# Kernel tuning notes

Hardware: AMD Instinct MI355X
Metric: run time of the kernel (lower is better)

Reference implementation:

```python
import jax, jax.numpy as jnp
import numpy as np

B, S, H = 32, 512, 2048
FP, SP = 1024, 1024


def setup_inputs() -> dict:
    key = jax.random.key(0)
    ks = jax.random.split(key, 8)
    X = jax.random.normal(ks[0], (B, S, H), dtype=jnp.float32)
    pY = jax.random.randint(ks[1], (B, S), 0, 3)
    # Y must be consistent with pY: hcw rows index [2, 2+FP), roo rows [2+FP, 2+FP+SP)
    y_hcw = jax.random.randint(ks[2], (B, S), 2, 2 + FP)
    y_roo = jax.random.randint(ks[3], (B, S), 2 + FP, 2 + FP + SP)
    Y = jnp.where(pY == 1, y_hcw, jnp.where(pY == 2, y_roo, 0))
    sc = 1.0 / np.sqrt(H)
    W_end = jax.random.normal(ks[4], (1, H), dtype=jnp.float32) * sc
    b_end = jnp.zeros((1,), jnp.float32)
    W_hcw = jax.random.normal(ks[5], (FP, H), dtype=jnp.float32) * sc
    b_hcw = jnp.zeros((FP,), jnp.float32)
    W_roo = jax.random.normal(ks[6], (SP, H), dtype=jnp.float32) * sc
    b_roo = jnp.zeros((SP,), jnp.float32)
    return {"X": X, "pY": pY, "Y": Y, "W_end": W_end, "b_end": b_end,
            "W_hcw": W_hcw, "b_hcw": b_hcw, "W_roo": W_roo, "b_roo": b_roo}


def reference(X, pY, Y, W_end, b_end, W_hcw, b_hcw, W_roo, b_roo):
    b, s, h = X.shape
    N = b * s
    Xf = X.reshape(N, h)
    pYf = pY.reshape(N)
    Yf = Y.reshape(N)

    end_mask = pYf == 0
    hcw_mask = pYf == 1
    roo_mask = pYf == 2

    # end head (Bernoulli prob)
    end_logit = Xf @ W_end.T + b_end            # [N, 1]
    end_prob = jax.nn.sigmoid(end_logit)[:, 0]  # [N]
    non_end = 1.0 - end_prob

    # hcw / roo heads: dense compute over all tokens, masked results match
    # the torch gather/scatter exactly at valid positions.
    P_hcw = jax.nn.softmax(Xf @ W_hcw.T + b_hcw, axis=-1)  # [N, FP]
    P_roo = jax.nn.softmax(Xf @ W_roo.T + b_roo, axis=-1)  # [N, SP]

    fp = W_hcw.shape[0]
    sp = W_roo.shape[0]
    idx_hcw = jnp.clip(Yf - 2, 0, fp - 1)
    idx_roo = jnp.clip(Yf - 2 - fp, 0, sp - 1)
    prob_hcw = jnp.take_along_axis(P_hcw, idx_hcw[:, None], axis=1)[:, 0]
    prob_roo = jnp.take_along_axis(P_roo, idx_roo[:, None], axis=1)[:, 0]

    prob = jnp.where(end_mask, end_prob,
                     jnp.where(hcw_mask, prob_hcw * non_end,
                               jnp.where(roo_mask, prob_roo * non_end, 1.0)))

    em = end_mask.astype(X.dtype)[:, None]
    hm = hcw_mask.astype(X.dtype)[:, None]
    rm = roo_mask.astype(X.dtype)[:, None]
    col_end = jnp.broadcast_to(end_prob[:, None], (N, 2)) * em        # [N, 2]
    col_hcw = P_hcw * non_end[:, None] * hm                           # [N, FP]
    col_roo = P_roo * non_end[:, None] * rm                           # [N, SP]
    prob_all_mat = jnp.concatenate([col_end, col_hcw, col_roo], axis=-1)

    log_prob = jnp.log(prob)
    return log_prob.reshape(b, s), prob_all_mat.reshape(b, s, fp + sp + 2)
```

## Files before the change

kernel.cpp:

```cpp
#include <hip/hip_runtime.h>
#include <hip/hip_bf16.h>
#include <cstddef>
#include <cstdint>

#define N_TOK 16384
#define H_    2048
#define FP_   1024
#define SP_   1024
#define C_    2050

#define BM 128
#define BN 128
#define BK 64
#define KP 72

typedef short bf16x8 __attribute__((ext_vector_type(8)));
typedef float f32x4  __attribute__((ext_vector_type(4)));
typedef float f4     __attribute__((ext_vector_type(4)));
typedef float f2     __attribute__((ext_vector_type(2)));

__device__ __forceinline__ unsigned pack_bf2(float a, float b) {
  __hip_bfloat16 x = __float2bfloat16(a);
  __hip_bfloat16 y = __float2bfloat16(b);
  unsigned short ux, uy;
  __builtin_memcpy(&ux, &x, 2);
  __builtin_memcpy(&uy, &y, 2);
  return (unsigned)ux | ((unsigned)uy << 16);
}

__device__ __forceinline__ unsigned short f2bf(float f) {
  __hip_bfloat16 h = __float2bfloat16(f);
  unsigned short u;
  __builtin_memcpy(&u, &h, 2);
  return u;
}

__device__ __forceinline__ float bf2f(unsigned short u) {
  unsigned v = (unsigned)u << 16;
  float f;
  __builtin_memcpy(&f, &v, 4);
  return f;
}

__global__ __launch_bounds__(256) void convert_kernel(
    const float* __restrict__ X,
    const float* __restrict__ W_hcw, const float* __restrict__ W_roo,
    const float* __restrict__ W_end, const float* __restrict__ b_end,
    unsigned short* __restrict__ Xb, unsigned short* __restrict__ Wb,
    float* __restrict__ mat)
{
  const int wave = threadIdx.x >> 6;
  const int lane = threadIdx.x & 63;
  const int row  = (blockIdx.x << 2) + wave;
  const bool isX = row < N_TOK;
  const float* src;
  unsigned short* dst;
  if (isX) {
    src = X + (size_t)row * H_;
    dst = Xb + (size_t)row * H_;
  } else {
    const int m = row - N_TOK;
    src = (m < FP_) ? (W_hcw + (size_t)m * H_) : (W_roo + (size_t)(m - FP_) * H_);
    dst = Wb + (size_t)m * H_;
  }
  float s = 0.f;
#pragma unroll
  for (int i = 0; i < 8; ++i) {
    const int e = (lane << 2) + (i << 8);
    f4 v = __builtin_nontemporal_load((const f4*)(src + e));
    uint2 p;
    p.x = pack_bf2(v[0], v[1]);
    p.y = pack_bf2(v[2], v[3]);
    *(uint2*)(dst + e) = p;
    if (isX) {
      float4 w = *(const float4*)(W_end + e);
      s += v[0] * w.x + v[1] * w.y + v[2] * w.z + v[3] * w.w;
    }
  }
  if (isX) {
#pragma unroll
    for (int o = 32; o; o >>= 1) s += __shfl_xor(s, o);
    if (lane == 0) mat[(size_t)row * C_] = s + b_end[0];
  }
}

__global__ __launch_bounds__(256) void gemm_lds_kernel(
    const unsigned short* __restrict__ Xb, const unsigned short* __restrict__ Wb,
    const float* __restrict__ b_hcw, const float* __restrict__ b_roo,
    float* __restrict__ mat)
{
  __shared__ __align__(16) unsigned short As[BM * BK];
  __shared__ __align__(16) unsigned short Bs[BN * BK];

  const int bid = blockIdx.x;
  const int xcd = bid & 7;
  const int loc = bid >> 3;
  const int c0 = (((xcd << 1) | (loc & 1))) * BN;
  const int n0 = (loc >> 1) * BM;
  const float* bias = (c0 < FP_) ? (b_hcw + c0) : (b_roo + (c0 - FP_));

  const int t    = threadIdx.x;
  const int wave = t >> 6;
  const int lane = t & 63;
  const int wy   = wave >> 1;
  const int wx   = wave & 1;
  const int quad = lane >> 4;
  const int l16  = lane & 15;

  const int srow   = t >> 3;
  const int gchunk = (t & 7) ^ (srow & 7);
  const unsigned short* gA = Xb + (size_t)(n0 + srow) * H_ + (gchunk << 3);
  const unsigned short* gB = Wb + (size_t)(c0 + srow) * H_ + (gchunk << 3);

  f32x4 acc[4][4];
#pragma unroll
  for (int i = 0; i < 4; ++i)
#pragma unroll
    for (int j = 0; j < 4; ++j)
#pragma unroll
      for (int r = 0; r < 4; ++r) acc[i][j][r] = 0.f;

  for (int k0 = 0; k0 < H_; k0 += BK) {
#pragma unroll
    for (int r = 0; r < 4; ++r) {
      __builtin_amdgcn_global_load_lds(
          (const __attribute__((address_space(1))) unsigned int*)(gA + (size_t)(r * 32) * H_ + k0),
          (__attribute__((address_space(3))) unsigned int*)(&As[(r * 32 + srow) * BK + ((t & 7) << 3)]),
          16, 0, 0);
      __builtin_amdgcn_global_load_lds(
          (const __attribute__((address_space(1))) unsigned int*)(gB + (size_t)(r * 32) * H_ + k0),
          (__attribute__((address_space(3))) unsigned int*)(&Bs[(r * 32 + srow) * BK + ((t & 7) << 3)]),
          16, 0, 0);
    }
    __syncthreads();

#pragma unroll
    for (int kk = 0; kk < 2; ++kk) {
      bf16x8 af[4], bfr[4];
      const int sw = l16 & 7;
#pragma unroll
      for (int i = 0; i < 4; ++i) {
        const int pos = ((kk << 2) + quad) ^ sw;
        af[i] = *(const bf16x8*)&As[(wy * 64 + i * 16 + l16) * BK + (pos << 3)];
      }
#pragma unroll
      for (int j = 0; j < 4; ++j) {
        const int pos = ((kk << 2) + quad) ^ sw;
        bfr[j] = *(const bf16x8*)&Bs[(wx * 64 + j * 16 + l16) * BK + (pos << 3)];
      }
#pragma unroll
      for (int i = 0; i < 4; ++i)
#pragma unroll
        for (int j = 0; j < 4; ++j)
          acc[i][j] = __builtin_amdgcn_mfma_f32_16x16x32_bf16(af[i], bfr[j], acc[i][j], 0, 0, 0);
    }
    __syncthreads();
  }

  float bj[4];
#pragma unroll
  for (int j = 0; j < 4; ++j) bj[j] = bias[wx * 64 + j * 16 + l16];
#pragma unroll
  for (int i = 0; i < 4; ++i) {
#pragma unroll
    for (int r = 0; r < 4; ++r) {
      const int row = n0 + wy * 64 + i * 16 + quad * 4 + r;
      unsigned short* dst =
          (unsigned short*)(mat + (size_t)row * C_ + 4) + c0 + wx * 64 + l16;
#pragma unroll
      for (int j = 0; j < 4; ++j) dst[j * 16] = f2bf(acc[i][j][r] + bj[j]);
    }
  }
}

__global__ __launch_bounds__(256) void end_head_kernel(
    const float* __restrict__ X, const float* __restrict__ W_end,
    const float* __restrict__ b_end, float* __restrict__ mat)
{
  const int wave = threadIdx.x >> 6;
  const int lane = threadIdx.x & 63;
  const int n = (blockIdx.x << 2) + wave;
  const float* x = X + (size_t)n * H_;
  float s = 0.f;
#pragma unroll
  for (int i = 0; i < 8; ++i) {
    const int e = (lane + (i << 6)) << 2;
    float4 xv = *(const float4*)(x + e);
    float4 wv = *(const float4*)(W_end + e);
    s += xv.x * wv.x + xv.y * wv.y + xv.z * wv.z + xv.w * wv.w;
  }
#pragma unroll
  for (int o = 32; o; o >>= 1) s += __shfl_xor(s, o);
  if (lane == 0) mat[(size_t)n * C_] = s + b_end[0];
}

__global__ __launch_bounds__(256) void logits_gemm_fused(
    const float* __restrict__ X,
    const float* __restrict__ W_hcw, const float* __restrict__ W_roo,
    const float* __restrict__ b_hcw, const float* __restrict__ b_roo,
    float* __restrict__ mat)
{
  __shared__ __align__(16) unsigned short As[BM * KP];
  __shared__ __align__(16) unsigned short Bs[BN * KP];

  const int c0 = blockIdx.x * BN;
  const int n0 = blockIdx.y * BM;
  const float* Wbase = (c0 < FP_) ? (W_hcw + (size_t)c0 * H_)
                                  : (W_roo + (size_t)(c0 - FP_) * H_);
  const float* bias  = (c0 < FP_) ? (b_hcw + c0) : (b_roo + (c0 - FP_));

  const int t    = threadIdx.x;
  const int wave = t >> 6;
  const int lane = t & 63;
  const int wy   = wave >> 1;
  const int wx   = wave & 1;
  const int quad = lane >> 4;
  const int l16  = lane & 15;
  const int tq = t & 3;
  const int tr = t >> 2;

  f32x4 acc[4][4];
#pragma unroll
  for (int i = 0; i < 4; ++i)
#pragma unroll
    for (int j = 0; j < 4; ++j)
#pragma unroll
      for (int r = 0; r < 4; ++r) acc[i][j][r] = 0.f;

  for (int k0 = 0; k0 < H_; k0 += BK) {
#pragma unroll
    for (int p = 0; p < 2; ++p) {
      const int row = tr + (p << 6);
      const float4* xs = (const float4*)(X + (size_t)(n0 + row) * H_ + k0 + (tq << 4));
      const float4* ws = (const float4*)(Wbase + (size_t)row * H_ + k0 + (tq << 4));
      float4 x0 = xs[0], x1 = xs[1], x2 = xs[2], x3 = xs[3];
      float4 w0 = ws[0], w1 = ws[1], w2 = ws[2], w3 = ws[3];
      uint4 ua0 = {pack_bf2(x0.x, x0.y), pack_bf2(x0.z, x0.w),
                   pack_bf2(x1.x, x1.y), pack_bf2(x1.z, x1.w)};
      uint4 ua1 = {pack_bf2(x2.x, x2.y), pack_bf2(x2.z, x2.w),
                   pack_bf2(x3.x, x3.y), pack_bf2(x3.z, x3.w)};
      uint4 ub0 = {pack_bf2(w0.x, w0.y), pack_bf2(w0.z, w0.w),
                   pack_bf2(w1.x, w1.y), pack_bf2(w1.z, w1.w)};
      uint4 ub1 = {pack_bf2(w2.x, w2.y), pack_bf2(w2.z, w2.w),
                   pack_bf2(w3.x, w3.y), pack_bf2(w3.z, w3.w)};
      *(uint4*)&As[row * KP + (tq << 4)]     = ua0;
      *(uint4*)&As[row * KP + (tq << 4) + 8] = ua1;
      *(uint4*)&Bs[row * KP + (tq << 4)]     = ub0;
      *(uint4*)&Bs[row * KP + (tq << 4) + 8] = ub1;
    }
    __syncthreads();
#pragma unroll
    for (int kk = 0; kk < 2; ++kk) {
      bf16x8 af[4], bfr[4];
#pragma unroll
      for (int i = 0; i < 4; ++i)
        af[i] = *(const bf16x8*)&As[(wy * 64 + i * 16 + l16) * KP + kk * 32 + quad * 8];
#pragma unroll
      for (int j = 0; j < 4; ++j)
        bfr[j] = *(const bf16x8*)&Bs[(wx * 64 + j * 16 + l16) * KP + kk * 32 + quad * 8];
#pragma unroll
      for (int i = 0; i < 4; ++i)
#pragma unroll
        for (int j = 0; j < 4; ++j)
          acc[i][j] = __builtin_amdgcn_mfma_f32_16x16x32_bf16(af[i], bfr[j], acc[i][j], 0, 0, 0);
    }
    __syncthreads();
  }

  float bj[4];
#pragma unroll
  for (int j = 0; j < 4; ++j) bj[j] = bias[wx * 64 + j * 16 + l16];
#pragma unroll
  for (int i = 0; i < 4; ++i) {
#pragma unroll
    for (int r = 0; r < 4; ++r) {
      const int row = n0 + wy * 64 + i * 16 + quad * 4 + r;
      unsigned short* dst =
          (unsigned short*)(mat + (size_t)row * C_ + 4) + c0 + wx * 64 + l16;
#pragma unroll
      for (int j = 0; j < 4; ++j) dst[j * 16] = f2bf(acc[i][j][r] + bj[j]);
    }
  }
}

__global__ __launch_bounds__(512) void epilogue_kernel(
    const int* __restrict__ pY, const int* __restrict__ Yf,
    float* __restrict__ logp, float* __restrict__ mat)
{
  const int w    = threadIdx.x >> 6;
  const int lane = threadIdx.x & 63;
  const int n    = (blockIdx.x << 3) + w;
  float* row = mat + (size_t)n * C_;
  const unsigned short* lg = (const unsigned short*)(row + 4);

  const int py = pY[n];
  const int y  = Yf[n];

  uint2 u[8];
#pragma unroll
  for (int i = 0; i < 8; ++i)
    u[i] = *(const uint2*)(lg + (i << 8) + (lane << 2));
  const float z = row[0];
  const int ih = min(max(y - 2, 0), FP_ - 1);
  const int ir = min(max(y - 2 - FP_, 0), SP_ - 1);
  const float lh = bf2f(lg[ih]);
  const float lr = bf2f(lg[FP_ + ir]);

  float e[32];
  float sh = 0.f, sr = 0.f;
#pragma unroll
  for (int i = 0; i < 8; ++i) {
    const float e0 = __expf(bf2f((unsigned short)(u[i].x & 0xffffu)));
    const float e1 = __expf(bf2f((unsigned short)(u[i].x >> 16)));
    const float e2 = __expf(bf2f((unsigned short)(u[i].y & 0xffffu)));
    const float e3 = __expf(bf2f((unsigned short)(u[i].y >> 16)));
    e[4 * i + 0] = e0; e[4 * i + 1] = e1; e[4 * i + 2] = e2; e[4 * i + 3] = e3;
    if (i < 4) sh += e0 + e1 + e2 + e3;
    else       sr += e0 + e1 + e2 + e3;
  }
#pragma unroll
  for (int o = 32; o; o >>= 1) sh += __shfl_xor(sh, o);
#pragma unroll
  for (int o = 32; o; o >>= 1) sr += __shfl_xor(sr, o);
  const float Sh = sh, Sr = sr;

  asm volatile("s_waitcnt vmcnt(0)" ::: "memory");

  const float sig = 1.f / (1.f + __expf(-z));
  const float ne  = 1.f - sig;
  const float sch = (py == 1) ? ne / Sh : 0.f;
  const float scr = (py == 2) ? ne / Sr : 0.f;
#pragma unroll
  for (int i = 0; i < 8; ++i) {
    const float sc = (i < 4) ? sch : scr;
    f2* wp = (f2*)(row + 2 + (i << 8) + (lane << 2));
    f2 v0 = {e[4 * i + 0] * sc, e[4 * i + 1] * sc};
    f2 v1 = {e[4 * i + 2] * sc, e[4 * i + 3] * sc};
    __builtin_nontemporal_store(v0, wp);
    __builtin_nontemporal_store(v1, wp + 1);
  }
  if (lane == 0) {
    const float ev = (py == 0) ? sig : 0.f;
    row[0] = ev;
    row[1] = ev;
    const float l1p   = log1pf(__expf(-fabsf(z)));
    const float sp_z  = fmaxf(z, 0.f)  + l1p;
    const float sp_mz = fmaxf(-z, 0.f) + l1p;
    float lp;
    if      (py == 0) lp = -sp_mz;
    else if (py == 1) lp = (lh - __logf(Sh)) - sp_z;
    else if (py == 2) lp = (lr - __logf(Sr)) - sp_z;
    else              lp = 0.f;
    logp[n] = lp;
  }
}

extern "C" void kernel_launch(void* const* d_in, const int* in_sizes, int n_in,
                              void* d_out, int out_size, void* d_ws, size_t ws_size,
                              hipStream_t stream) {
  const float* X     = (const float*)d_in[0];
  const int*   pY    = (const int*)  d_in[1];
  const int*   Y     = (const int*)  d_in[2];
  const float* W_end = (const float*)d_in[3];
  const float* b_end = (const float*)d_in[4];
  const float* W_hcw = (const float*)d_in[5];
  const float* b_hcw = (const float*)d_in[6];
  const float* W_roo = (const float*)d_in[7];
  const float* b_roo = (const float*)d_in[8];

  float* out  = (float*)d_out;
  float* logp = out;
  float* mat  = out + N_TOK;

  const size_t xb_bytes = (size_t)N_TOK * H_ * 2;
  const size_t wb_bytes = (size_t)(FP_ + SP_) * H_ * 2;

  if (ws_size >= xb_bytes + wb_bytes) {
    unsigned short* Xb = (unsigned short*)d_ws;
    unsigned short* Wb = (unsigned short*)((char*)d_ws + xb_bytes);
    convert_kernel<<<(N_TOK + FP_ + SP_) / 4, 256, 0, stream>>>(
        X, W_hcw, W_roo, W_end, b_end, Xb, Wb, mat);
    gemm_lds_kernel<<<2048, 256, 0, stream>>>(Xb, Wb, b_hcw, b_roo, mat);
  } else {
    dim3 g(2048 / BN, N_TOK / BM);
    end_head_kernel<<<N_TOK / 4, 256, 0, stream>>>(X, W_end, b_end, mat);
    logits_gemm_fused<<<g, 256, 0, stream>>>(X, W_hcw, W_roo, b_hcw, b_roo, mat);
  }
  epilogue_kernel<<<N_TOK / 8, 512, 0, stream>>>(pY, Y, logp, mat);
}
```

Baseline: 417.2 us.

## Fuse softmax epilogue into GEMM via per-row-tile atomic ticket

The separate epilogue kernel is folded into the GEMM. Each block increments an atomic counter stored in an unused output slot of its row tile, and the last of the 16 column blocks for that tile runs the softmax, scaling and log-prob computation for its 128 rows. This removes a kernel launch and lets the epilogue start while other tiles are still in the GEMM. In exchange it serialises the epilogue work onto one block per row tile and depends on threadfence ordering and on the counter being zeroed by the convert kernel.

```diff
diff --git a/kernel.cpp b/kernel.cpp
--- a/kernel.cpp
+++ b/kernel.cpp
@@ -80,17 +80,22 @@
   if (isX) {
 #pragma unroll
     for (int o = 32; o; o >>= 1) s += __shfl_xor(s, o);
-    if (lane == 0) mat[(size_t)row * C_] = s + b_end[0];
+    if (lane == 0) {
+      mat[(size_t)row * C_] = s + b_end[0];
+      if ((row & 127) == 0) mat[(size_t)row * C_ + 1] = 0.0f;
+    }
   }
 }
 
 __global__ __launch_bounds__(256) void gemm_lds_kernel(
     const unsigned short* __restrict__ Xb, const unsigned short* __restrict__ Wb,
     const float* __restrict__ b_hcw, const float* __restrict__ b_roo,
-    float* __restrict__ mat)
+    const int* __restrict__ pY, const int* __restrict__ Yf,
+    float* __restrict__ logp, float* __restrict__ mat)
 {
   __shared__ __align__(16) unsigned short As[BM * BK];
   __shared__ __align__(16) unsigned short Bs[BN * BK];
+  __shared__ int ticket_s;
 
   const int bid = blockIdx.x;
   const int xcd = bid & 7;
@@ -169,6 +174,82 @@
           (unsigned short*)(mat + (size_t)row * C_ + 4) + c0 + wx * 64 + l16;
 #pragma unroll
       for (int j = 0; j < 4; ++j) dst[j * 16] = f2bf(acc[i][j][r] + bj[j]);
+    }
+  }
+
+  __threadfence();
+  __syncthreads();
+  if (t == 0)
+    ticket_s = atomicAdd((int*)(mat + (size_t)n0 * C_ + 1), 1);
+  __syncthreads();
+  if (ticket_s != 15) return;
+
+  __threadfence();
+  const int n_base = n0 + wave * 32;
+  for (int it = 0; it < 32; ++it) {
+    const int n = n_base + it;
+    float* row = mat + (size_t)n * C_;
+    const unsigned short* lg = (const unsigned short*)(row + 4);
+
+    const int py = pY[n];
+    const int y  = Yf[n];
+    const float z = row[0];
+    const int ih = min(max(y - 2, 0), FP_ - 1);
+    const int ir = min(max(y - 2 - FP_, 0), SP_ - 1);
+    const float lh = bf2f(lg[ih]);
+    const float lr = bf2f(lg[FP_ + ir]);
+
+    uint2 u[8];
+#pragma unroll
+    for (int i = 0; i < 8; ++i)
+      u[i] = *(const uint2*)(lg + (i << 8) + (lane << 2));
+
+    float e[32];
+    float sh = 0.f, sr = 0.f;
+#pragma unroll
+    for (int i = 0; i < 8; ++i) {
+      const float e0 = __expf(bf2f((unsigned short)(u[i].x & 0xffffu)));
+      const float e1 = __expf(bf2f((unsigned short)(u[i].x >> 16)));
+      const float e2 = __expf(bf2f((unsigned short)(u[i].y & 0xffffu)));
+      const float e3 = __expf(bf2f((unsigned short)(u[i].y >> 16)));
+      e[4 * i + 0] = e0; e[4 * i + 1] = e1; e[4 * i + 2] = e2; e[4 * i + 3] = e3;
+      if (i < 4) sh += e0 + e1 + e2 + e3;
+      else       sr += e0 + e1 + e2 + e3;
+    }
+#pragma unroll
+    for (int o = 32; o; o >>= 1) sh += __shfl_xor(sh, o);
+#pragma unroll
+    for (int o = 32; o; o >>= 1) sr += __shfl_xor(sr, o);
+    const float Sh = sh, Sr = sr;
+
+    asm volatile("s_waitcnt vmcnt(0)" ::: "memory");
+
+    const float sig = 1.f / (1.f + __expf(-z));
+    const float ne  = 1.f - sig;
+    const float sch = (py == 1) ? ne / Sh : 0.f;
+    const float scr = (py == 2) ? ne / Sr : 0.f;
+#pragma unroll
+    for (int i = 0; i < 8; ++i) {
+      const float sc = (i < 4) ? sch : scr;
+      f2* wp = (f2*)(row + 2 + (i << 8) + (lane << 2));
+      f2 v0 = {e[4 * i + 0] * sc, e[4 * i + 1] * sc};
+      f2 v1 = {e[4 * i + 2] * sc, e[4 * i + 3] * sc};
+      __builtin_nontemporal_store(v0, wp);
+      __builtin_nontemporal_store(v1, wp + 1);
+    }
+    if (lane == 0) {
+      const float ev = (py == 0) ? sig : 0.f;
+      row[0] = ev;
+      row[1] = ev;
+      const float l1p   = log1pf(__expf(-fabsf(z)));
+      const float sp_z  = fmaxf(z, 0.f)  + l1p;
+      const float sp_mz = fmaxf(-z, 0.f) + l1p;
+      float lp;
+      if      (py == 0) lp = -sp_mz;
+      else if (py == 1) lp = (lh - __logf(Sh)) - sp_z;
+      else if (py == 2) lp = (lr - __logf(Sr)) - sp_z;
+      else              lp = 0.f;
+      logp[n] = lp;
     }
   }
 }
@@ -380,11 +461,12 @@
     unsigned short* Wb = (unsigned short*)((char*)d_ws + xb_bytes);
     convert_kernel<<<(N_TOK + FP_ + SP_) / 4, 256, 0, stream>>>(
         X, W_hcw, W_roo, W_end, b_end, Xb, Wb, mat);
-    gemm_lds_kernel<<<2048, 256, 0, stream>>>(Xb, Wb, b_hcw, b_roo, mat);
+    gemm_lds_kernel<<<2048, 256, 0, stream>>>(
+        Xb, Wb, b_hcw, b_roo, pY, Y, logp, mat);
   } else {
     dim3 g(2048 / BN, N_TOK / BM);
     end_head_kernel<<<N_TOK / 4, 256, 0, stream>>>(X, W_end, b_end, mat);
     logits_gemm_fused<<<g, 256, 0, stream>>>(X, W_hcw, W_roo, b_hcw, b_roo, mat);
-  }
-  epilogue_kernel<<<N_TOK / 8, 512, 0, stream>>>(pY, Y, logp, mat);
-}
+    epilogue_kernel<<<N_TOK / 8, 512, 0, stream>>>(pY, Y, logp, mat);
+  }
+}
```

Result: slower. 1.090 ms (+161.4%).

## Fuse fp32-to-bf16 conversion of X into the GEMM A-tile load

Applied to the files above, without the earlier changes.

Removes the separate bf16 copy of X from the convert kernel and workspace. The GEMM now reads fp32 X directly, packs it to bf16 in registers and stores it to LDS, while W still uses async global-to-LDS loads. This avoids writing and re-reading a large intermediate buffer. In exchange the GEMM reads twice as many bytes for A, and those loads are synchronous register round-trips rather than direct-to-LDS.

```diff
diff --git a/kernel.cpp b/kernel.cpp
--- a/kernel.cpp
+++ b/kernel.cpp
@@ -46,46 +46,44 @@
     const float* __restrict__ X,
     const float* __restrict__ W_hcw, const float* __restrict__ W_roo,
     const float* __restrict__ W_end, const float* __restrict__ b_end,
-    unsigned short* __restrict__ Xb, unsigned short* __restrict__ Wb,
+    unsigned short* __restrict__ Wb,
     float* __restrict__ mat)
 {
   const int wave = threadIdx.x >> 6;
   const int lane = threadIdx.x & 63;
   const int row  = (blockIdx.x << 2) + wave;
-  const bool isX = row < N_TOK;
-  const float* src;
-  unsigned short* dst;
-  if (isX) {
-    src = X + (size_t)row * H_;
-    dst = Xb + (size_t)row * H_;
+  if (row < N_TOK) {
+    const float* src = X + (size_t)row * H_;
+    float s = 0.f;
+#pragma unroll
+    for (int i = 0; i < 8; ++i) {
+      const int e = (lane << 2) + (i << 8);
+      float4 v = *(const float4*)(src + e);
+      float4 w = *(const float4*)(W_end + e);
+      s += v.x * w.x + v.y * w.y + v.z * w.z + v.w * w.w;
+    }
+#pragma unroll
+    for (int o = 32; o; o >>= 1) s += __shfl_xor(s, o);
+    if (lane == 0) mat[(size_t)row * C_] = s + b_end[0];
   } else {
     const int m = row - N_TOK;
-    src = (m < FP_) ? (W_hcw + (size_t)m * H_) : (W_roo + (size_t)(m - FP_) * H_);
-    dst = Wb + (size_t)m * H_;
-  }
-  float s = 0.f;
-#pragma unroll
-  for (int i = 0; i < 8; ++i) {
-    const int e = (lane << 2) + (i << 8);
-    f4 v = __builtin_nontemporal_load((const f4*)(src + e));
-    uint2 p;
-    p.x = pack_bf2(v[0], v[1]);
-    p.y = pack_bf2(v[2], v[3]);
-    *(uint2*)(dst + e) = p;
-    if (isX) {
-      float4 w = *(const float4*)(W_end + e);
-      s += v[0] * w.x + v[1] * w.y + v[2] * w.z + v[3] * w.w;
-    }
-  }
-  if (isX) {
-#pragma unroll
-    for (int o = 32; o; o >>= 1) s += __shfl_xor(s, o);
-    if (lane == 0) mat[(size_t)row * C_] = s + b_end[0];
+    const float* src = (m < FP_) ? (W_hcw + (size_t)m * H_)
+                                 : (W_roo + (size_t)(m - FP_) * H_);
+    unsigned short* dst = Wb + (size_t)m * H_;
+#pragma unroll
+    for (int i = 0; i < 8; ++i) {
+      const int e = (lane << 2) + (i << 8);
+      f4 v = __builtin_nontemporal_load((const f4*)(src + e));
+      uint2 p;
+      p.x = pack_bf2(v[0], v[1]);
+      p.y = pack_bf2(v[2], v[3]);
+      *(uint2*)(dst + e) = p;
+    }
   }
 }
 
 __global__ __launch_bounds__(256) void gemm_lds_kernel(
-    const unsigned short* __restrict__ Xb, const unsigned short* __restrict__ Wb,
+    const float* __restrict__ X, const unsigned short* __restrict__ Wb,
     const float* __restrict__ b_hcw, const float* __restrict__ b_roo,
     float* __restrict__ mat)
 {
@@ -109,8 +107,9 @@
 
   const int srow   = t >> 3;
   const int gchunk = (t & 7) ^ (srow & 7);
-  const unsigned short* gA = Xb + (size_t)(n0 + srow) * H_ + (gchunk << 3);
-  const unsigned short* gB = Wb + (size_t)(c0 + srow) * H_ + (gchunk << 3);
+  const float*          gAf = X  + (size_t)(n0 + srow) * H_ + (gchunk << 3);
+  const unsigned short* gB  = Wb + (size_t)(c0 + srow) * H_ + (gchunk << 3);
+  const int aslot = srow * BK + ((t & 7) << 3);
 
   f32x4 acc[4][4];
 #pragma unroll
@@ -124,13 +123,18 @@
 #pragma unroll
     for (int r = 0; r < 4; ++r) {
       __builtin_amdgcn_global_load_lds(
-          (const __attribute__((address_space(1))) unsigned int*)(gA + (size_t)(r * 32) * H_ + k0),
-          (__attribute__((address_space(3))) unsigned int*)(&As[(r * 32 + srow) * BK + ((t & 7) << 3)]),
+          (const __attribute__((address_space(1))) unsigned int*)(gB + (size_t)(r * 32) * H_ + k0),
+          (__attribute__((address_space(3))) unsigned int*)(&Bs[r * 32 * BK + aslot]),
           16, 0, 0);
-      __builtin_amdgcn_global_load_lds(
-          (const __attribute__((address_space(1))) unsigned int*)(gB + (size_t)(r * 32) * H_ + k0),
-          (__attribute__((address_space(3))) unsigned int*)(&Bs[(r * 32 + srow) * BK + ((t & 7) << 3)]),
-          16, 0, 0);
+    }
+#pragma unroll
+    for (int r = 0; r < 4; ++r) {
+      const float* p = gAf + (size_t)(r * 32) * H_ + k0;
+      float4 x0 = *(const float4*)(p);
+      float4 x1 = *(const float4*)(p + 4);
+      uint4 ua = {pack_bf2(x0.x, x0.y), pack_bf2(x0.z, x0.w),
+                  pack_bf2(x1.x, x1.y), pack_bf2(x1.z, x1.w)};
+      *(uint4*)&As[r * 32 * BK + aslot] = ua;
     }
     __syncthreads();
 
@@ -372,15 +376,13 @@
   float* logp = out;
   float* mat  = out + N_TOK;
 
-  const size_t xb_bytes = (size_t)N_TOK * H_ * 2;
   const size_t wb_bytes = (size_t)(FP_ + SP_) * H_ * 2;
 
-  if (ws_size >= xb_bytes + wb_bytes) {
-    unsigned short* Xb = (unsigned short*)d_ws;
-    unsigned short* Wb = (unsigned short*)((char*)d_ws + xb_bytes);
+  if (ws_size >= wb_bytes) {
+    unsigned short* Wb = (unsigned short*)d_ws;
     convert_kernel<<<(N_TOK + FP_ + SP_) / 4, 256, 0, stream>>>(
-        X, W_hcw, W_roo, W_end, b_end, Xb, Wb, mat);
-    gemm_lds_kernel<<<2048, 256, 0, stream>>>(Xb, Wb, b_hcw, b_roo, mat);
+        X, W_hcw, W_roo, W_end, b_end, Wb, mat);
+    gemm_lds_kernel<<<2048, 256, 0, stream>>>(X, Wb, b_hcw, b_roo, mat);
   } else {
     dim3 g(2048 / BN, N_TOK / BM);
     end_head_kernel<<<N_TOK / 4, 256, 0, stream>>>(X, W_end, b_end, mat);
```

Result: slower. 456.5 us (+9.4%).
